# Optimization experiments

Hardware: AMD Instinct MI355X
Metric: run time of the kernel (lower is better)

Reference implementation:

```python
import jax, jax.numpy as jnp
import numpy as np

D_MODEL = 1024
N_HEADS = 16
D_K = D_MODEL // N_HEADS
NEG = -1e9


def setup_inputs() -> dict:
    key = jax.random.key(0)
    ks = jax.random.split(key, 10)
    B, S = 4, 2048
    x = jax.random.normal(ks[0], (B, S, D_MODEL), dtype=jnp.float32)
    mask = jax.random.randint(ks[1], (B, S, S), 0, 2).astype(jnp.bool_)
    sc = 1.0 / np.sqrt(D_MODEL)
    Wq = jax.random.normal(ks[2], (D_MODEL, D_MODEL), dtype=jnp.float32) * sc
    bq = jnp.zeros((D_MODEL,), dtype=jnp.float32)
    Wk = jax.random.normal(ks[3], (D_MODEL, D_MODEL), dtype=jnp.float32) * sc
    bk = jnp.zeros((D_MODEL,), dtype=jnp.float32)
    Wv = jax.random.normal(ks[4], (D_MODEL, D_MODEL), dtype=jnp.float32) * sc
    bv = jnp.zeros((D_MODEL,), dtype=jnp.float32)
    Wo = jax.random.normal(ks[5], (D_MODEL, D_MODEL), dtype=jnp.float32) * sc
    bo = jnp.zeros((D_MODEL,), dtype=jnp.float32)
    return {"x": x, "mask": mask, "Wq": Wq, "bq": bq, "Wk": Wk, "bk": bk,
            "Wv": Wv, "bv": bv, "Wo": Wo, "bo": bo}


def _split_heads(t, B, S):
    # [B,S,d_model] -> [B,H,S,d_k]
    return t.reshape(B, S, N_HEADS, D_K).transpose(0, 2, 1, 3)


def reference(x, mask, Wq, bq, Wk, bk, Wv, bv, Wo, bo):
    B, S, _ = x.shape
    Q = _split_heads(x @ Wq + bq, B, S)
    K = _split_heads(x @ Wk + bk, B, S)
    V = _split_heads(x @ Wv + bv, B, S)
    scale = jnp.sqrt(jnp.float32(D_K))
    scores = jnp.einsum('bhqd,bhkd->bhqk', Q, K) / scale
    scores = jnp.where(mask[:, None, :, :], jnp.float32(NEG), scores)
    attn = jax.nn.softmax(scores, axis=-1)
    ctx = jnp.einsum('bhqk,bhkd->bhqd', attn, V)
    ctx = ctx.transpose(0, 2, 1, 3).reshape(B, S, D_MODEL)
    return ctx @ Wo + bo
```

## Files before the change

kernel.cpp:

```cpp
#include <hip/hip_runtime.h>

#define D_MODEL 1024
#define N_HEADS 16
#define D_K     64
#define BATCH   4
#define SEQ     2048
#define MROWS   (BATCH * SEQ)
#define QSCALE  0.18033688011112042f

typedef __bf16 bf16x8 __attribute__((ext_vector_type(8)));
typedef float  f32x4  __attribute__((ext_vector_type(4)));
typedef float  f32x16 __attribute__((ext_vector_type(16)));
typedef unsigned short ushort8 __attribute__((ext_vector_type(8)));
typedef unsigned short ushort4v __attribute__((ext_vector_type(4)));

#if __has_builtin(__builtin_amdgcn_exp2f)
#define EXP2F(x) __builtin_amdgcn_exp2f(x)
#else
#define EXP2F(x) exp2f(x)
#endif

__device__ inline unsigned short f2bf(float f) {
    union { float f; unsigned int u; } v; v.f = f;
    unsigned int u = v.u;
    unsigned int r = (u + 0x7fffu + ((u >> 16) & 1u)) >> 16;
    return (unsigned short)r;
}

__device__ inline void load_lds16(const void* g, void* l) {
    __builtin_amdgcn_global_load_lds(
        (const __attribute__((address_space(1))) unsigned int*)g,
        (__attribute__((address_space(3))) unsigned int*)l, 16, 0, 0);
}

__global__ __launch_bounds__(256) void wprep(const float* __restrict__ Wq,
                                             const float* __restrict__ Wk,
                                             const float* __restrict__ Wv,
                                             const float* __restrict__ Wo,
                                             unsigned short* __restrict__ wt) {
    __shared__ __align__(16) unsigned short t[64][65];
    int w  = blockIdx.z;
    const float* W = (w == 0) ? Wq : (w == 1) ? Wk : (w == 2) ? Wv : Wo;
    int k0 = blockIdx.x * 64, n0 = blockIdx.y * 64;
    int tid = threadIdx.x;
    int nl = tid & 63, kq = tid >> 6;
#pragma unroll
    for (int i = 0; i < 16; i++) {
        int kl = kq * 16 + i;
        t[kl][nl] = f2bf(W[(size_t)(k0 + kl) * D_MODEL + n0 + nl]);
    }
    __syncthreads();
    unsigned short* out = wt + (size_t)w * D_MODEL * D_MODEL;
#pragma unroll
    for (int p = 0; p < 2; p++) {
        int nrow = p * 32 + (tid >> 3);
        int c8   = (tid & 7) * 8;
        ushort8 o;
#pragma unroll
        for (int j = 0; j < 8; j++) o[j] = t[c8 + j][nrow];
        *reinterpret_cast<ushort8*>(out + (size_t)(n0 + nrow) * D_MODEL + k0 + c8) = o;
    }
}

__global__ __launch_bounds__(256) void xprep(const float4* __restrict__ x,
                                             unsigned short* __restrict__ xb) {
    int i = blockIdx.x * 256 + threadIdx.x;
    float4 v = x[i];
    ushort4v o;
    o[0] = f2bf(v.x); o[1] = f2bf(v.y); o[2] = f2bf(v.z); o[3] = f2bf(v.w);
    *reinterpret_cast<ushort4v*>(xb + (size_t)i * 4) = o;
}

__global__ __launch_bounds__(256) void mprep(const int* __restrict__ mask,
                                             unsigned long long* __restrict__ mb) {
    int row = blockIdx.x;
    int tid = threadIdx.x;
    int wv  = tid >> 6;
#pragma unroll
    for (int w = 0; w < 8; w++) {
        int col = w * 256 + tid;
        int mval = mask[(size_t)row * SEQ + col];
        unsigned long long bits = __ballot(mval != 0);
        if ((tid & 63) == 0) mb[(size_t)row * 32 + w * 4 + wv] = bits;
    }
}

__global__ __launch_bounds__(256) void qkv_gemm(const unsigned short* __restrict__ xb,
                                                const unsigned short* __restrict__ wt,
                                                const float* __restrict__ bq,
                                                const float* __restrict__ bk,
                                                const float* __restrict__ bvv,
                                                unsigned short* __restrict__ qb,
                                                unsigned short* __restrict__ kb,
                                                unsigned short* __restrict__ vt) {
    __shared__ __align__(16) unsigned short lds_a[128 * 32];
    __shared__ __align__(16) unsigned short lds_b[128 * 32];
    int tid = threadIdx.x;
    int wave = tid >> 6, lane = tid & 63;
    int c = lane & 15, g = lane >> 4;
    int wave_m = (wave & 1) * 64, wave_n = (wave >> 1) * 64;
    int nblk = blockIdx.x * 128, mblk = blockIdx.y * 128;

    int oct0 = wave * 128 + lane, oct1 = oct0 + 64;
    int ra0 = oct0 >> 2, ga0 = ((oct0 & 3) ^ (ra0 & 3)) * 8;
    int ra1 = oct1 >> 2, ga1 = ((oct1 & 3) ^ (ra1 & 3)) * 8;
    const unsigned short* pa0 = xb + (size_t)(mblk + ra0) * D_MODEL + ga0;
    const unsigned short* pa1 = xb + (size_t)(mblk + ra1) * D_MODEL + ga1;
    const unsigned short* pb0 = wt + (size_t)(nblk + ra0) * D_MODEL + ga0;
    const unsigned short* pb1 = wt + (size_t)(nblk + ra1) * D_MODEL + ga1;
    unsigned short* la0 = lds_a + wave * 1024;
    unsigned short* la1 = la0 + 512;
    unsigned short* lb0 = lds_b + wave * 1024;
    unsigned short* lb1 = lb0 + 512;

    int aoff[4], boff[4];
#pragma unroll
    for (int mi = 0; mi < 4; mi++) {
        int row = wave_m + mi * 16 + c;
        aoff[mi] = (row * 4 + (g ^ (row & 3))) * 16;
    }
#pragma unroll
    for (int ni = 0; ni < 4; ni++) {
        int row = wave_n + ni * 16 + c;
        boff[ni] = (row * 4 + (g ^ (row & 3))) * 16;
    }

    f32x4 acc[4][4];
#pragma unroll
    for (int mi = 0; mi < 4; mi++)
#pragma unroll
        for (int ni = 0; ni < 4; ni++) acc[mi][ni] = f32x4{0.f, 0.f, 0.f, 0.f};

    for (int k0 = 0; k0 < D_MODEL; k0 += 32) {
        load_lds16(pa0 + k0, la0);
        load_lds16(pa1 + k0, la1);
        load_lds16(pb0 + k0, lb0);
        load_lds16(pb1 + k0, lb1);
        __syncthreads();
        bf16x8 af[4], bfr[4];
#pragma unroll
        for (int mi = 0; mi < 4; mi++)
            af[mi] = *reinterpret_cast<const bf16x8*>(reinterpret_cast<const char*>(lds_a) + aoff[mi]);
#pragma unroll
        for (int ni = 0; ni < 4; ni++)
            bfr[ni] = *reinterpret_cast<const bf16x8*>(reinterpret_cast<const char*>(lds_b) + boff[ni]);
#pragma unroll
        for (int mi = 0; mi < 4; mi++)
#pragma unroll
            for (int ni = 0; ni < 4; ni++)
                acc[mi][ni] = __builtin_amdgcn_mfma_f32_16x16x32_bf16(af[mi], bfr[ni], acc[mi][ni], 0, 0, 0);
        __syncthreads();
    }

    int nb = nblk + wave_n;
    int wsel = nb >> 10;
    int h = (nb >> 6) & 15;
    int dk0 = nb & 63;
    int mglob = mblk + wave_m;
    int b = mglob >> 11;
    int s0 = mglob & (SEQ - 1);
    size_t bh = (size_t)(b * N_HEADS + h);
    const float* bias = (wsel == 0) ? bq : (wsel == 1) ? bk : bvv;
    int nn = nb & (D_MODEL - 1);
    float bval[4];
#pragma unroll
    for (int ni = 0; ni < 4; ni++) bval[ni] = bias[nn + ni * 16 + c];
    float oscale = (wsel == 0) ? QSCALE : 1.0f;

    if (wsel < 2) {
        unsigned short* outp = wsel ? kb : qb;
#pragma unroll
        for (int mi = 0; mi < 4; mi++)
#pragma unroll
            for (int ni = 0; ni < 4; ni++) {
                int dk = dk0 + ni * 16 + c;
#pragma unroll
                for (int r = 0; r < 4; r++) {
                    int s = s0 + mi * 16 + g * 4 + r;
                    outp[(bh * SEQ + s) * 64 + dk] = f2bf((acc[mi][ni][r] + bval[ni]) * oscale);
                }
            }
    } else {
#pragma unroll
        for (int mi = 0; mi < 4; mi++)
#pragma unroll
            for (int ni = 0; ni < 4; ni++) {
                int dk = dk0 + ni * 16 + c;
                int s = s0 + mi * 16 + g * 4;
                ushort4v o;
#pragma unroll
                for (int r = 0; r < 4; r++) o[r] = f2bf(acc[mi][ni][r] + bval[ni]);
                *reinterpret_cast<ushort4v*>(vt + (bh * 64 + dk) * SEQ + s) = o;
            }
    }
}

__global__ __launch_bounds__(128, 2) void attn(const unsigned short* __restrict__ qb,
                                               const unsigned short* __restrict__ kb,
                                               const unsigned short* __restrict__ vt,
                                               const unsigned long long* __restrict__ mb,
                                               unsigned short* __restrict__ ctx) {
    __shared__ __align__(16) unsigned char smem[36864];
    unsigned short* lk = (unsigned short*)smem;
    unsigned short* lv = (unsigned short*)(smem + 8192);
    unsigned int*  lpA = (unsigned int*)(smem + 16384);

    int tid = threadIdx.x;
    int wave = tid >> 6, lane = tid & 63;
    int q31 = lane & 31, hi = lane >> 5;
    int bh = blockIdx.x >> 4;
    int q0 = (blockIdx.x & 15) * 128 + wave * 64;
    int b = bh >> 4, h = bh & 15;
    const unsigned short* qbase = qb + (size_t)bh * SEQ * 64;
    const unsigned short* kbase = kb + (size_t)bh * SEQ * 64;
    const unsigned short* vbase = vt + (size_t)bh * 64 * SEQ;
    const unsigned long long* mp0 = mb + ((size_t)b * SEQ + q0 + q31) * 32;
    const unsigned long long* mp1 = mp0 + 1024;

    bf16x8 qf[2][4];
#pragma unroll
    for (int t = 0; t < 2; t++) {
        const unsigned short* qr = qbase + (size_t)(q0 + 32 * t + q31) * 64 + hi * 8;
#pragma unroll
        for (int c = 0; c < 4; c++)
            qf[t][c] = *reinterpret_cast<const bf16x8*>(qr + c * 16);
    }

    int srow = lane >> 3;
    int soct = (lane & 7) ^ srow;
    const unsigned short* ksrc[4];
    const unsigned short* vsrc[4];
    unsigned short* klb[4];
    unsigned short* vlb[4];
#pragma unroll
    for (int i = 0; i < 4; i++) {
        int rbase = 16 * i + 8 * wave;
        ksrc[i] = kbase + (size_t)(rbase + srow) * 64 + soct * 8;
        vsrc[i] = vbase + (size_t)(rbase + srow) * SEQ + soct * 8;
        klb[i] = lk + rbase * 64;
        vlb[i] = lv + rbase * 64;
    }

    int kofs[2][4];
#pragma unroll
    for (int s = 0; s < 2; s++)
#pragma unroll
        for (int c = 0; c < 4; c++)
            kofs[s][c] = (32 * s + q31) * 128 + (((hi + 2 * c) ^ (q31 & 7)) * 16);

    unsigned int* lp = lpA + wave * 2560 + q31 * 20;

    float lsum[2] = {0.f, 0.f};
    f32x16 po[2][2];
#pragma unroll
    for (int i = 0; i < 16; i++) {
        po[0][0][i] = 0.f; po[0][1][i] = 0.f;
        po[1][0][i] = 0.f; po[1][1][i] = 0.f;
    }

    for (int it = 0; it < SEQ / 64; it++) {
#pragma unroll
        for (int i = 0; i < 4; i++) {
            load_lds16(ksrc[i] + it * 4096, klb[i]);
            load_lds16(vsrc[i] + it * 64, vlb[i]);
        }
        unsigned long long w64[2];
        w64[0] = mp0[it];
        w64[1] = mp1[it];
        __syncthreads();

        const char* lkb = (const char*)lk;
        const char* lvb = (const char*)lv;

#pragma unroll
        for (int s = 0; s < 2; s++) {
            f32x16 sq[2];
#pragma unroll
            for (int i = 0; i < 16; i++) { sq[0][i] = 0.f; sq[1][i] = 0.f; }
#pragma unroll
            for (int c = 0; c < 4; c++) {
                bf16x8 kf = *reinterpret_cast<const bf16x8*>(lkb + kofs[s][c]);
                sq[0] = __builtin_amdgcn_mfma_f32_32x32x16_bf16(kf, qf[0][c], sq[0], 0, 0, 0);
                sq[1] = __builtin_amdgcn_mfma_f32_32x32x16_bf16(kf, qf[1][c], sq[1], 0, 0, 0);
            }
#pragma unroll
            for (int t = 0; t < 2; t++) {
                unsigned int wt_ = ~(unsigned int)(w64[t] >> (32 * s));
                unsigned int* pw = lp + (t * 2 + s) * 640;
#pragma unroll
                for (int j = 0; j < 4; j++) {
                    unsigned int nj = wt_ >> (8 * j + 4 * hi);
                    unsigned int t0, t1, t2, t3;
                    {
                        float p = EXP2F(sq[t][4 * j + 0]);
                        unsigned int m = (unsigned int)((int)(nj << 31) >> 31);
                        t0 = __float_as_uint(p) & m; lsum[t] += __uint_as_float(t0);
                    }
                    {
                        float p = EXP2F(sq[t][4 * j + 1]);
                        unsigned int m = (unsigned int)((int)(nj << 30) >> 31);
                        t1 = __float_as_uint(p) & m; lsum[t] += __uint_as_float(t1);
                    }
                    {
                        float p = EXP2F(sq[t][4 * j + 2]);
                        unsigned int m = (unsigned int)((int)(nj << 29) >> 31);
                        t2 = __float_as_uint(p) & m; lsum[t] += __uint_as_float(t2);
                    }
                    {
                        float p = EXP2F(sq[t][4 * j + 3]);
                        unsigned int m = (unsigned int)((int)(nj << 28) >> 31);
                        t3 = __float_as_uint(p) & m; lsum[t] += __uint_as_float(t3);
                    }
                    uint2 u;
                    u.x = (t0 >> 16) | (t1 & 0xFFFF0000u);
                    u.y = (t2 >> 16) | (t3 & 0xFFFF0000u);
                    *reinterpret_cast<uint2*>(pw + 4 * j + 2 * hi) = u;
                }
            }
#pragma unroll
            for (int cp = 0; cp < 2; cp++) {
                int c = 2 * s + cp;
                union { bf16x8 v; uint4 u; } pb0, pb1;
                pb0.u = *reinterpret_cast<const uint4*>(lp + (0 * 2 + s) * 640 + 8 * cp + 4 * hi);
                pb1.u = *reinterpret_cast<const uint4*>(lp + (1 * 2 + s) * 640 + 8 * cp + 4 * hi);
#pragma unroll
                for (int so = 0; so < 2; so++) {
                    bf16x8 vf = *reinterpret_cast<const bf16x8*>(lvb + kofs[so][c]);
                    po[0][so] = __builtin_amdgcn_mfma_f32_32x32x16_bf16(vf, pb0.v, po[0][so], 0, 0, 0);
                    po[1][so] = __builtin_amdgcn_mfma_f32_32x32x16_bf16(vf, pb1.v, po[1][so], 0, 0, 0);
                }
            }
        }
        __syncthreads();
    }

    float inv[2];
#pragma unroll
    for (int t = 0; t < 2; t++) {
        lsum[t] += __shfl_xor(lsum[t], 32);
        inv[t] = 1.f / lsum[t];
    }

    unsigned int* ob = (unsigned int*)(smem + wave * 8192);
    int csw = 4 * (q31 & 7);
#pragma unroll
    for (int t = 0; t < 2; t++) {
        unsigned int* obr = ob + (32 * t + q31) * 32;
#pragma unroll
        for (int so = 0; so < 2; so++)
#pragma unroll
            for (int j = 0; j < 4; j++) {
                unsigned int w0 = (unsigned int)f2bf(po[t][so][4 * j + 0] * inv[t])
                                | ((unsigned int)f2bf(po[t][so][4 * j + 1] * inv[t]) << 16);
                unsigned int w1 = (unsigned int)f2bf(po[t][so][4 * j + 2] * inv[t])
                                | ((unsigned int)f2bf(po[t][so][4 * j + 3] * inv[t]) << 16);
                int d = (16 * so + 4 * j + 2 * hi) ^ csw;
                uint2 u; u.x = w0; u.y = w1;
                *reinterpret_cast<uint2*>(obr + d) = u;
            }
    }
    __builtin_amdgcn_s_waitcnt(0);
    size_t crow = (size_t)b * SEQ + q0;
    int o = lane & 7, rl = lane >> 3;
#pragma unroll
    for (int i = 0; i < 8; i++) {
        int r = 8 * i + rl;
        uint4 v = *reinterpret_cast<const uint4*>(ob + r * 32 + 4 * (o ^ (r & 7)));
        *reinterpret_cast<uint4*>(ctx + (crow + r) * D_MODEL + h * 64 + o * 8) = v;
    }
}

__global__ __launch_bounds__(256) void oproj(const unsigned short* __restrict__ ctx,
                                             const unsigned short* __restrict__ wt,
                                             const float* __restrict__ bo,
                                             float* __restrict__ out) {
    __shared__ __align__(16) unsigned short lds_a[128 * 32];
    __shared__ __align__(16) unsigned short lds_b[128 * 32];
    int tid = threadIdx.x;
    int wave = tid >> 6, lane = tid & 63;
    int c = lane & 15, g = lane >> 4;
    int wave_m = (wave & 1) * 64, wave_n = (wave >> 1) * 64;
    int nblk = blockIdx.x * 128, mblk = blockIdx.y * 128;
    const unsigned short* wo = wt + (size_t)3 * D_MODEL * D_MODEL;

    int oct0 = wave * 128 + lane, oct1 = oct0 + 64;
    int ra0 = oct0 >> 2, ga0 = ((oct0 & 3) ^ (ra0 & 3)) * 8;
    int ra1 = oct1 >> 2, ga1 = ((oct1 & 3) ^ (ra1 & 3)) * 8;
    const unsigned short* pa0 = ctx + (size_t)(mblk + ra0) * D_MODEL + ga0;
    const unsigned short* pa1 = ctx + (size_t)(mblk + ra1) * D_MODEL + ga1;
    const unsigned short* pb0 = wo + (size_t)(nblk + ra0) * D_MODEL + ga0;
    const unsigned short* pb1 = wo + (size_t)(nblk + ra1) * D_MODEL + ga1;
    unsigned short* la0 = lds_a + wave * 1024;
    unsigned short* la1 = la0 + 512;
    unsigned short* lb0 = lds_b + wave * 1024;
    unsigned short* lb1 = lb0 + 512;

    int aoff[4], boff[4];
#pragma unroll
    for (int mi = 0; mi < 4; mi++) {
        int row = wave_m + mi * 16 + c;
        aoff[mi] = (row * 4 + (g ^ (row & 3))) * 16;
    }
#pragma unroll
    for (int ni = 0; ni < 4; ni++) {
        int row = wave_n + ni * 16 + c;
        boff[ni] = (row * 4 + (g ^ (row & 3))) * 16;
    }

    f32x4 acc[4][4];
#pragma unroll
    for (int mi = 0; mi < 4; mi++)
#pragma unroll
        for (int ni = 0; ni < 4; ni++) acc[mi][ni] = f32x4{0.f, 0.f, 0.f, 0.f};

    for (int k0 = 0; k0 < D_MODEL; k0 += 32) {
        load_lds16(pa0 + k0, la0);
        load_lds16(pa1 + k0, la1);
        load_lds16(pb0 + k0, lb0);
        load_lds16(pb1 + k0, lb1);
        __syncthreads();
        bf16x8 af[4], bfr[4];
#pragma unroll
        for (int mi = 0; mi < 4; mi++)
            af[mi] = *reinterpret_cast<const bf16x8*>(reinterpret_cast<const char*>(lds_a) + aoff[mi]);
#pragma unroll
        for (int ni = 0; ni < 4; ni++)
            bfr[ni] = *reinterpret_cast<const bf16x8*>(reinterpret_cast<const char*>(lds_b) + boff[ni]);
#pragma unroll
        for (int mi = 0; mi < 4; mi++)
#pragma unroll
            for (int ni = 0; ni < 4; ni++)
                acc[mi][ni] = __builtin_amdgcn_mfma_f32_16x16x32_bf16(af[mi], bfr[ni], acc[mi][ni], 0, 0, 0);
        __syncthreads();
    }

    float bval[4];
#pragma unroll
    for (int ni = 0; ni < 4; ni++) bval[ni] = bo[nblk + wave_n + ni * 16 + c];
#pragma unroll
    for (int mi = 0; mi < 4; mi++)
#pragma unroll
        for (int ni = 0; ni < 4; ni++) {
            int n = nblk + wave_n + ni * 16 + c;
#pragma unroll
            for (int r = 0; r < 4; r++) {
                int m = mblk + wave_m + mi * 16 + g * 4 + r;
                out[(size_t)m * D_MODEL + n] = acc[mi][ni][r] + bval[ni];
            }
        }
}

extern "C" void kernel_launch(void* const* d_in, const int* in_sizes, int n_in,
                              void* d_out, int out_size, void* d_ws, size_t ws_size,
                              hipStream_t stream) {
    const float* x    = (const float*)d_in[0];
    const int*   mask = (const int*)d_in[1];
    const float* Wq = (const float*)d_in[2];
    const float* bq = (const float*)d_in[3];
    const float* Wk = (const float*)d_in[4];
    const float* bk = (const float*)d_in[5];
    const float* Wv = (const float*)d_in[6];
    const float* bv = (const float*)d_in[7];
    const float* Wo = (const float*)d_in[8];
    const float* bo = (const float*)d_in[9];
    float* out = (float*)d_out;

    char* ws = (char*)d_ws;
    const size_t MB = 1024 * 1024;
    unsigned short* wt  = (unsigned short*)(ws + 0 * MB);
    unsigned short* xb  = (unsigned short*)(ws + 8 * MB);
    unsigned short* qb  = (unsigned short*)(ws + 24 * MB);
    unsigned short* kb  = (unsigned short*)(ws + 40 * MB);
    unsigned short* vt  = (unsigned short*)(ws + 56 * MB);
    unsigned short* ctx = (unsigned short*)(ws + 72 * MB);
    unsigned long long* mb = (unsigned long long*)(ws + 88 * MB);

    wprep<<<dim3(16, 16, 4), 256, 0, stream>>>(Wq, Wk, Wv, Wo, wt);
    xprep<<<dim3(MROWS * D_MODEL / 4 / 256), 256, 0, stream>>>((const float4*)x, xb);
    mprep<<<dim3(MROWS), 256, 0, stream>>>(mask, mb);
    qkv_gemm<<<dim3(24, 64), 256, 0, stream>>>(xb, wt, bq, bk, bv, qb, kb, vt);
    attn<<<dim3(1024), 128, 0, stream>>>(qb, kb, vt, mb, ctx);
    oproj<<<dim3(8, 64), 256, 0, stream>>>(ctx, wt, bo, out);
}
```

Before: 376.8 us.

## Split attention over the key dimension and merge partials in a combine kernel

The attention kernel now splits the key sequence into two halves, launching twice as many blocks. Each block writes unnormalized bf16 partial context plus row sums, and a new combine kernel adds the partials and normalizes them. The LDS footprint is halved and the occupancy hint raised from 2 to 3 blocks per CU, with the goal of more parallelism and better latency hiding. The cost is an extra kernel pass over the context and an extra bf16 rounding of the unnormalized partials. The second partial buffer reuses the xb workspace, and combine writes in place to ctx.

New measurement: 499.5 us. +32.6%, slower.

```diff
diff --git a/kernel.cpp b/kernel.cpp
--- a/kernel.cpp
+++ b/kernel.cpp
@@ -195,12 +195,14 @@
     }
 }
 
-__global__ __launch_bounds__(128, 2) void attn(const unsigned short* __restrict__ qb,
+__global__ __launch_bounds__(128, 3) void attn(const unsigned short* __restrict__ qb,
                                                const unsigned short* __restrict__ kb,
                                                const unsigned short* __restrict__ vt,
                                                const unsigned long long* __restrict__ mb,
-                                               unsigned short* __restrict__ ctx) {
-    __shared__ __align__(16) unsigned char smem[36864];
+                                               unsigned short* __restrict__ pp0,
+                                               unsigned short* __restrict__ pp1,
+                                               float* __restrict__ lsw) {
+    __shared__ __align__(16) unsigned char smem[26624];
     unsigned short* lk = (unsigned short*)smem;
     unsigned short* lv = (unsigned short*)(smem + 8192);
     unsigned int*  lpA = (unsigned int*)(smem + 16384);
@@ -208,13 +210,15 @@
     int tid = threadIdx.x;
     int wave = tid >> 6, lane = tid & 63;
     int q31 = lane & 31, hi = lane >> 5;
-    int bh = blockIdx.x >> 4;
-    int q0 = (blockIdx.x & 15) * 128 + wave * 64;
+    int ks = blockIdx.x & 1;
+    int qblk = (blockIdx.x >> 1) & 15;
+    int bh = blockIdx.x >> 5;
+    int q0 = qblk * 128 + wave * 64;
     int b = bh >> 4, h = bh & 15;
     const unsigned short* qbase = qb + (size_t)bh * SEQ * 64;
     const unsigned short* kbase = kb + (size_t)bh * SEQ * 64;
     const unsigned short* vbase = vt + (size_t)bh * 64 * SEQ;
-    const unsigned long long* mp0 = mb + ((size_t)b * SEQ + q0 + q31) * 32;
+    const unsigned long long* mp0 = mb + ((size_t)b * SEQ + q0 + q31) * 32 + ks * 16;
     const unsigned long long* mp1 = mp0 + 1024;
 
     bf16x8 qf[2][4];
@@ -235,8 +239,8 @@
 #pragma unroll
     for (int i = 0; i < 4; i++) {
         int rbase = 16 * i + 8 * wave;
-        ksrc[i] = kbase + (size_t)(rbase + srow) * 64 + soct * 8;
-        vsrc[i] = vbase + (size_t)(rbase + srow) * SEQ + soct * 8;
+        ksrc[i] = kbase + (size_t)(rbase + srow) * 64 + soct * 8 + (size_t)ks * 1024 * 64;
+        vsrc[i] = vbase + (size_t)(rbase + srow) * SEQ + soct * 8 + ks * 1024;
         klb[i] = lk + rbase * 64;
         vlb[i] = lv + rbase * 64;
     }
@@ -248,7 +252,7 @@
         for (int c = 0; c < 4; c++)
             kofs[s][c] = (32 * s + q31) * 128 + (((hi + 2 * c) ^ (q31 & 7)) * 16);
 
-    unsigned int* lp = lpA + wave * 2560 + q31 * 20;
+    unsigned int* lp = lpA + wave * 1280 + q31 * 20;
 
     float lsum[2] = {0.f, 0.f};
     f32x16 po[2][2];
@@ -258,7 +262,7 @@
         po[1][0][i] = 0.f; po[1][1][i] = 0.f;
     }
 
-    for (int it = 0; it < SEQ / 64; it++) {
+    for (int it = 0; it < 16; it++) {
 #pragma unroll
         for (int i = 0; i < 4; i++) {
             load_lds16(ksrc[i] + it * 4096, klb[i]);
@@ -286,7 +290,7 @@
 #pragma unroll
             for (int t = 0; t < 2; t++) {
                 unsigned int wt_ = ~(unsigned int)(w64[t] >> (32 * s));
-                unsigned int* pw = lp + (t * 2 + s) * 640;
+                unsigned int* pw = lp + t * 640;
 #pragma unroll
                 for (int j = 0; j < 4; j++) {
                     unsigned int nj = wt_ >> (8 * j + 4 * hi);
@@ -321,8 +325,8 @@
             for (int cp = 0; cp < 2; cp++) {
                 int c = 2 * s + cp;
                 union { bf16x8 v; uint4 u; } pb0, pb1;
-                pb0.u = *reinterpret_cast<const uint4*>(lp + (0 * 2 + s) * 640 + 8 * cp + 4 * hi);
-                pb1.u = *reinterpret_cast<const uint4*>(lp + (1 * 2 + s) * 640 + 8 * cp + 4 * hi);
+                pb0.u = *reinterpret_cast<const uint4*>(lp + 0 * 640 + 8 * cp + 4 * hi);
+                pb1.u = *reinterpret_cast<const uint4*>(lp + 1 * 640 + 8 * cp + 4 * hi);
 #pragma unroll
                 for (int so = 0; so < 2; so++) {
                     bf16x8 vf = *reinterpret_cast<const bf16x8*>(lvb + kofs[so][c]);
@@ -334,11 +338,14 @@
         __syncthreads();
     }
 
-    float inv[2];
-#pragma unroll
-    for (int t = 0; t < 2; t++) {
-        lsum[t] += __shfl_xor(lsum[t], 32);
-        inv[t] = 1.f / lsum[t];
+    float ls[2];
+#pragma unroll
+    for (int t = 0; t < 2; t++)
+        ls[t] = lsum[t] + __shfl_xor(lsum[t], 32);
+    if (hi == 0) {
+        int base = ks * (64 * SEQ) + bh * SEQ + q0;
+        lsw[base + q31]      = ls[0];
+        lsw[base + 32 + q31] = ls[1];
     }
 
     unsigned int* ob = (unsigned int*)(smem + wave * 8192);
@@ -350,24 +357,47 @@
         for (int so = 0; so < 2; so++)
 #pragma unroll
             for (int j = 0; j < 4; j++) {
-                unsigned int w0 = (unsigned int)f2bf(po[t][so][4 * j + 0] * inv[t])
-                                | ((unsigned int)f2bf(po[t][so][4 * j + 1] * inv[t]) << 16);
-                unsigned int w1 = (unsigned int)f2bf(po[t][so][4 * j + 2] * inv[t])
-                                | ((unsigned int)f2bf(po[t][so][4 * j + 3] * inv[t]) << 16);
+                unsigned int w0 = (unsigned int)f2bf(po[t][so][4 * j + 0])
+                                | ((unsigned int)f2bf(po[t][so][4 * j + 1]) << 16);
+                unsigned int w1 = (unsigned int)f2bf(po[t][so][4 * j + 2])
+                                | ((unsigned int)f2bf(po[t][so][4 * j + 3]) << 16);
                 int d = (16 * so + 4 * j + 2 * hi) ^ csw;
                 uint2 u; u.x = w0; u.y = w1;
                 *reinterpret_cast<uint2*>(obr + d) = u;
             }
     }
     __builtin_amdgcn_s_waitcnt(0);
+    unsigned short* pp = ks ? pp1 : pp0;
     size_t crow = (size_t)b * SEQ + q0;
     int o = lane & 7, rl = lane >> 3;
 #pragma unroll
     for (int i = 0; i < 8; i++) {
         int r = 8 * i + rl;
         uint4 v = *reinterpret_cast<const uint4*>(ob + r * 32 + 4 * (o ^ (r & 7)));
-        *reinterpret_cast<uint4*>(ctx + (crow + r) * D_MODEL + h * 64 + o * 8) = v;
-    }
+        *reinterpret_cast<uint4*>(pp + (crow + r) * D_MODEL + h * 64 + o * 8) = v;
+    }
+}
+
+__global__ __launch_bounds__(256) void combine(const unsigned short* __restrict__ p0,
+                                               const unsigned short* __restrict__ p1,
+                                               const float* __restrict__ lsw,
+                                               unsigned short* __restrict__ outp) {
+    int i = blockIdx.x * 256 + threadIdx.x;
+    int row = i >> 7;
+    int col8 = i & 127;
+    int b = row >> 11, s = row & 2047, h = col8 >> 3;
+    int bhq = (((b << 4) + h) << 11) + s;
+    float inv = 1.f / (lsw[bhq] + lsw[64 * SEQ + bhq]);
+    ushort8 a = *reinterpret_cast<const ushort8*>(p0 + (size_t)i * 8);
+    ushort8 c = *reinterpret_cast<const ushort8*>(p1 + (size_t)i * 8);
+    ushort8 o;
+#pragma unroll
+    for (int j = 0; j < 8; j++) {
+        float fa = __uint_as_float((unsigned int)a[j] << 16);
+        float fc = __uint_as_float((unsigned int)c[j] << 16);
+        o[j] = f2bf((fa + fc) * inv);
+    }
+    *reinterpret_cast<ushort8*>(outp + (size_t)i * 8) = o;
 }
 
 __global__ __launch_bounds__(256) void oproj(const unsigned short* __restrict__ ctx,
@@ -474,11 +504,13 @@
     unsigned short* vt  = (unsigned short*)(ws + 56 * MB);
     unsigned short* ctx = (unsigned short*)(ws + 72 * MB);
     unsigned long long* mb = (unsigned long long*)(ws + 88 * MB);
+    float* lsw = (float*)(ws + 90 * MB);
 
     wprep<<<dim3(16, 16, 4), 256, 0, stream>>>(Wq, Wk, Wv, Wo, wt);
     xprep<<<dim3(MROWS * D_MODEL / 4 / 256), 256, 0, stream>>>((const float4*)x, xb);
     mprep<<<dim3(MROWS), 256, 0, stream>>>(mask, mb);
     qkv_gemm<<<dim3(24, 64), 256, 0, stream>>>(xb, wt, bq, bk, bv, qb, kb, vt);
-    attn<<<dim3(1024), 128, 0, stream>>>(qb, kb, vt, mb, ctx);
+    attn<<<dim3(2048), 128, 0, stream>>>(qb, kb, vt, mb, ctx, xb, lsw);
+    combine<<<dim3(MROWS * D_MODEL / 8 / 256), 256, 0, stream>>>(ctx, xb, lsw, ctx);
     oproj<<<dim3(8, 64), 256, 0, stream>>>(ctx, wt, bo, out);
 }
```
